# Optimization experiments

Measured on AMD Instinct MI355X. Metric: run time of the kernel, lower is better.

## Reference

```python
import jax, jax.numpy as jnp
import numpy as np

N_NODES = 50000
N_EDGES = 800000
IN_DIM = 128
OUT_DIM = 128
NUM_HEADS = 8
HEAD_DIM = OUT_DIM // NUM_HEADS
LN_EPS = 1e-5


def setup_inputs() -> dict:
    key = jax.random.key(0)
    ks = jax.random.split(key, 8)
    # xavier-uniform bounds
    def xavier(k, shape, fan_in, fan_out):
        a = float(np.sqrt(6.0 / (fan_in + fan_out)))
        return jax.random.uniform(k, shape, jnp.float32, -a, a)
    x = jax.random.normal(ks[0], (N_NODES, IN_DIM), jnp.float32)
    edge_index = jax.random.randint(ks[1], (2, N_EDGES), 0, N_NODES, jnp.int32)
    # store Linear weights as (in, out) so forward is x @ W (same math as torch x @ W.T)
    W_src = xavier(ks[2], (IN_DIM, OUT_DIM), IN_DIM, OUT_DIM)
    W_dst = xavier(ks[3], (IN_DIM, OUT_DIM), IN_DIM, OUT_DIM)
    attn = xavier(ks[4], (NUM_HEADS, HEAD_DIM), HEAD_DIM, NUM_HEADS)
    W_out = xavier(ks[5], (OUT_DIM, OUT_DIM), OUT_DIM, OUT_DIM)
    b_out = jnp.zeros((OUT_DIM,), jnp.float32)
    gamma = jnp.ones((OUT_DIM,), jnp.float32)
    beta = jnp.zeros((OUT_DIM,), jnp.float32)
    return {"x": x, "edge_index": edge_index, "W_src": W_src, "W_dst": W_dst,
            "attn": attn, "W_out": W_out, "b_out": b_out, "gamma": gamma, "beta": beta}


def reference(x, edge_index, W_src, W_dst, attn, W_out, b_out, gamma, beta):
    N = x.shape[0]
    H, D = attn.shape
    src, dst = edge_index[0], edge_index[1]
    # node transforms: (N, H, D)
    h_src = (x @ W_src).reshape(N, H, D)
    h_dst = (x @ W_dst).reshape(N, H, D)
    # per-edge GATv2 attention logits (E, H)
    h_src_e = h_src[src]                                  # (E, H, D)
    e = jax.nn.leaky_relu(h_src_e + h_dst[dst], 0.2)
    s = jnp.einsum('ehd,hd->eh', e, attn)
    # segment (scatter) softmax over incoming edges of each dst node
    m = jax.ops.segment_max(s, dst, num_segments=N)       # (N, H)
    exp = jnp.exp(s - m[dst])
    denom = jax.ops.segment_sum(exp, dst, num_segments=N)
    alpha = exp / (denom[dst] + 1e-8)                     # (E, H)
    # weighted message aggregation
    msg = (h_src_e * alpha[..., None]).reshape(-1, H * D)
    out = jax.ops.segment_sum(msg, dst, num_segments=N)   # (N, H*D)
    out = out @ W_out + b_out
    out = out + x                                          # residual (in_dim == out_dim)
    # LayerNorm
    mu = jnp.mean(out, axis=-1, keepdims=True)
    var = jnp.var(out, axis=-1, keepdims=True)
    out = (out - mu) * jax.lax.rsqrt(var + LN_EPS) * gamma + beta
    return out
```

## Files before the change

### kernel.cpp

```cpp
#include <hip/hip_runtime.h>
#include <hip/hip_bf16.h>

#define HEADS 8
#define CDIM 128
#define CAP 96
#define CHUNK 2048
#define LOG2E 1.44269504088896f

typedef __attribute__((ext_vector_type(8))) short bf16x8;
typedef __attribute__((ext_vector_type(4))) float f32x4;
typedef __attribute__((ext_vector_type(2))) _Float16 h16x2;

__device__ __forceinline__ unsigned short f2bs(float f) {
    union { __hip_bfloat16 b; unsigned short u; } c;
    c.b = __float2bfloat16(f);
    return c.u;
}

__device__ __forceinline__ unsigned short f2hs(float f) {
    union { _Float16 h; unsigned short u; } c;
    c.h = (_Float16)f;
    return c.u;
}

__global__ __launch_bounds__(256) void prep_kernel(
        const int* __restrict__ ei,
        int* __restrict__ cnt,
        int* __restrict__ bucket,
        const float* __restrict__ Wsrc,
        const float* __restrict__ Wdst,
        const float* __restrict__ Wout,
        unsigned short* __restrict__ WT,
        unsigned short* __restrict__ WoT, int E, int nedgeblk) {
    const int b = blockIdx.x;
    if (b < nedgeblk) {
        const int shard = b & 7;
        const int base = (b >> 3) * CHUNK;
        int end = base + CHUNK; if (end > E) end = E;
        for (int e = base + (int)threadIdx.x; e < end; e += 256) {
            const int dst = ei[E + e];
            if ((dst & 7) == shard) {
                const int src = ei[e];
                const int pos = atomicAdd(&cnt[dst], 1);
                if (pos < CAP) bucket[(size_t)dst * CAP + pos] = src;
            }
        }
        return;
    }
    int i = (b - nedgeblk) * 256 + threadIdx.x;
    if (i < 16384)      { WT[i] = f2bs(Wsrc[(i & 127) * CDIM + (i >> 7)]); }
    else if (i < 32768) { int j = i - 16384; WT[16384 + j] = f2bs(Wdst[(j & 127) * CDIM + (j >> 7)]); }
    else if (i < 49152) { int j = i - 32768; WoT[j] = f2bs(Wout[(j & 127) * CDIM + (j >> 7)]); }
}

__global__ __launch_bounds__(256) void transform_mfma64f(
        const float* __restrict__ x,
        const unsigned short* __restrict__ WT,
        unsigned short* __restrict__ hsrc,
        unsigned short* __restrict__ hdst, int N) {
    __shared__ unsigned short As[64][136];
    __shared__ unsigned short Bs[128][136];
    const int t = threadIdx.x;
    const int m0 = blockIdx.x * 64;
    for (int i = t; i < 64 * 32; i += 256) {
        const int r = i >> 5, kq = i & 31;
        const int gr = m0 + r;
        float4 v = make_float4(0.f, 0.f, 0.f, 0.f);
        if (gr < N) v = *(const float4*)(x + (size_t)gr * CDIM + kq * 4);
        uint2 pk;
        pk.x = (unsigned)f2bs(v.x) | ((unsigned)f2bs(v.y) << 16);
        pk.y = (unsigned)f2bs(v.z) | ((unsigned)f2bs(v.w) << 16);
        *(uint2*)&As[r][kq * 4] = pk;
    }
    const int w = t >> 6, lane = t & 63, l16 = lane & 15, quad = lane >> 4;
    const int wm = (w & 1) * 32, wn = (w >> 1) * 64;
#pragma unroll
    for (int half = 0; half < 2; half++) {
        const unsigned short* Wb = WT + (size_t)half * 16384;
        for (int i = t; i < 128 * 16; i += 256) {
            const int r = i >> 4, q = i & 15;
            *(uint4*)&Bs[r][q * 8] = *(const uint4*)(Wb + (size_t)r * CDIM + q * 8);
        }
        __syncthreads();
        f32x4 acc[2][4];
#pragma unroll
        for (int mi = 0; mi < 2; mi++)
#pragma unroll
            for (int ni = 0; ni < 4; ni++) acc[mi][ni] = (f32x4){0.f, 0.f, 0.f, 0.f};
#pragma unroll
        for (int kc = 0; kc < 4; kc++) {
            const int k0 = kc * 32 + quad * 8;
            bf16x8 af[2], bf[4];
            af[0] = *(const bf16x8*)&As[wm + l16][k0];
            af[1] = *(const bf16x8*)&As[wm + 16 + l16][k0];
#pragma unroll
            for (int ni = 0; ni < 4; ni++)
                bf[ni] = *(const bf16x8*)&Bs[wn + ni * 16 + l16][k0];
#pragma unroll
            for (int mi = 0; mi < 2; mi++)
#pragma unroll
                for (int ni = 0; ni < 4; ni++)
                    acc[mi][ni] = __builtin_amdgcn_mfma_f32_16x16x32_bf16(af[mi], bf[ni], acc[mi][ni], 0, 0, 0);
        }
        unsigned short* H = half ? hdst : hsrc;
#pragma unroll
        for (int mi = 0; mi < 2; mi++)
#pragma unroll
            for (int reg = 0; reg < 4; reg++) {
                const int gm = m0 + wm + mi * 16 + quad * 4 + reg;
                if (gm < N) {
#pragma unroll
                    for (int ni = 0; ni < 4; ni++)
                        H[(size_t)gm * CDIM + wn + ni * 16 + l16] = f2hs(acc[mi][ni][reg]);
                }
            }
        __syncthreads();
    }
}

__global__ __launch_bounds__(256) void attn_agg6(
        const unsigned short* __restrict__ hsrc,
        const unsigned short* __restrict__ hdst,
        const float* __restrict__ attn,
        const int* __restrict__ cnt,
        const int* __restrict__ bucket,
        unsigned short* __restrict__ aggb) {
    __shared__ int src_lds[4][CAP];
    const int t = threadIdx.x;
    const int w = t >> 6, lane = t & 63;
    const int dst = blockIdx.x * 4 + w;
    int deg = cnt[dst];
    deg = deg > CAP ? CAP : deg;
    for (int j = lane; j < deg; j += 64)
        src_lds[w][j] = bucket[(size_t)dst * CAP + j];

    const int l32 = lane & 31;
    const int eh = lane >> 5;
    const uint2 hdu = *(const uint2*)(hdst + (size_t)dst * CDIM + l32 * 4);
    const h16x2 hd01 = __builtin_bit_cast(h16x2, hdu.x);
    const h16x2 hd23 = __builtin_bit_cast(h16x2, hdu.y);
    const float4 a4 = ((const float4*)attn)[l32];
    h16x2 a01, a23;
    a01[0] = (_Float16)(a4.x * LOG2E); a01[1] = (_Float16)(a4.y * LOG2E);
    a23[0] = (_Float16)(a4.z * LOG2E); a23[1] = (_Float16)(a4.w * LOG2E);
    const h16x2 k02 = { (_Float16)0.2f, (_Float16)0.2f };

    const unsigned short* hb = hsrc + l32 * 4;

    float l = 0.f, acc0 = 0.f, acc1 = 0.f, acc2 = 0.f, acc3 = 0.f;
    for (int j0 = 0; j0 < deg; j0 += 8) {
        uint2 vv[4];
#pragma unroll
        for (int p = 0; p < 4; p++) {
            const int j = j0 + 2 * p + eh;
            const int sj = (j < deg) ? src_lds[w][j] : 0;
            vv[p] = *(const uint2*)(hb + (size_t)sj * CDIM);
        }
#pragma unroll
        for (int p = 0; p < 4; p++) {
            const int j = j0 + 2 * p + eh;
            const h16x2 v01 = __builtin_bit_cast(h16x2, vv[p].x);
            const h16x2 v23 = __builtin_bit_cast(h16x2, vv[p].y);
            h16x2 e01 = v01 + hd01;
            h16x2 e23 = v23 + hd23;
            e01 = __builtin_elementwise_max(e01, e01 * k02);
            e23 = __builtin_elementwise_max(e23, e23 * k02);
            float pp = __builtin_amdgcn_fdot2(e01, a01, 0.f, false);
            pp = __builtin_amdgcn_fdot2(e23, a23, pp, false);
            pp += __int_as_float(__builtin_amdgcn_update_dpp(0, __float_as_int(pp), 0xB1, 0xF, 0xF, true));
            pp += __int_as_float(__builtin_amdgcn_update_dpp(0, __float_as_int(pp), 0x4E, 0xF, 0xF, true));
            float wgt = __builtin_amdgcn_exp2f(pp);
            wgt = (j < deg) ? wgt : 0.f;
            l += wgt;
            acc0 = fmaf(wgt, (float)v01[0], acc0);
            acc1 = fmaf(wgt, (float)v01[1], acc1);
            acc2 = fmaf(wgt, (float)v23[0], acc2);
            acc3 = fmaf(wgt, (float)v23[1], acc3);
        }
    }
    l    += __shfl_xor(l, 32);
    acc0 += __shfl_xor(acc0, 32);
    acc1 += __shfl_xor(acc1, 32);
    acc2 += __shfl_xor(acc2, 32);
    acc3 += __shfl_xor(acc3, 32);
    if (lane < 32) {
        const float r = 1.f / (l + 1e-8f);
        uint2 o;
        o.x = (unsigned)f2bs(acc0 * r) | ((unsigned)f2bs(acc1 * r) << 16);
        o.y = (unsigned)f2bs(acc2 * r) | ((unsigned)f2bs(acc3 * r) << 16);
        *(uint2*)(aggb + (size_t)dst * CDIM + l32 * 4) = o;
    }
}

__global__ __launch_bounds__(256) void out_mfma_ln64(
        const unsigned short* __restrict__ aggb,
        const float* __restrict__ x,
        const unsigned short* __restrict__ WoT,
        const float* __restrict__ bo,
        const float* __restrict__ gam,
        const float* __restrict__ bet,
        float* __restrict__ out, int N) {
    __shared__ unsigned short As[64][136];
    __shared__ unsigned short Bs[128][136];
    __shared__ float red1[64][2], red2[64][2];
    __shared__ float s_mu[64], s_rs[64];
    const int t = threadIdx.x;
    const int m0 = blockIdx.x * 64;
    for (int i = t; i < 64 * 16; i += 256) {
        const int r = i >> 4, q = i & 15;
        const int gr = m0 + r;
        uint4 v = make_uint4(0u, 0u, 0u, 0u);
        if (gr < N) v = *(const uint4*)(aggb + (size_t)gr * CDIM + q * 8);
        *(uint4*)&As[r][q * 8] = v;
    }
    for (int i = t; i < 128 * 16; i += 256) {
        const int r = i >> 4, q = i & 15;
        *(uint4*)&Bs[r][q * 8] = *(const uint4*)(WoT + (size_t)r * CDIM + q * 8);
    }
    __syncthreads();
    const int w = t >> 6, lane = t & 63, l16 = lane & 15, quad = lane >> 4;
    const int wm = (w & 1) * 32, wn = (w >> 1) * 64;
    f32x4 acc[2][4];
#pragma unroll
    for (int mi = 0; mi < 2; mi++)
#pragma unroll
        for (int ni = 0; ni < 4; ni++) acc[mi][ni] = (f32x4){0.f, 0.f, 0.f, 0.f};
#pragma unroll
    for (int kc = 0; kc < 4; kc++) {
        const int k0 = kc * 32 + quad * 8;
        bf16x8 af[2], bf[4];
        af[0] = *(const bf16x8*)&As[l16 + wm][k0];
        af[1] = *(const bf16x8*)&As[l16 + wm + 16][k0];
#pragma unroll
        for (int ni = 0; ni < 4; ni++)
            bf[ni] = *(const bf16x8*)&Bs[wn + ni * 16 + l16][k0];
#pragma unroll
        for (int mi = 0; mi < 2; mi++)
#pragma unroll
            for (int ni = 0; ni < 4; ni++)
                acc[mi][ni] = __builtin_amdgcn_mfma_f32_16x16x32_bf16(af[mi], bf[ni], acc[mi][ni], 0, 0, 0);
    }
    float bi[4], g4[4], be4[4];
#pragma unroll
    for (int ni = 0; ni < 4; ni++) {
        const int n = wn + ni * 16 + l16;
        bi[ni] = bo[n]; g4[ni] = gam[n]; be4[ni] = bet[n];
    }
#pragma unroll
    for (int mi = 0; mi < 2; mi++)
#pragma unroll
        for (int reg = 0; reg < 4; reg++) {
            const int gm = m0 + wm + mi * 16 + quad * 4 + reg;
#pragma unroll
            for (int ni = 0; ni < 4; ni++) {
                const float xr = (gm < N) ? x[(size_t)gm * CDIM + wn + ni * 16 + l16] : 0.f;
                acc[mi][ni][reg] += bi[ni] + xr;
            }
        }
#pragma unroll
    for (int mi = 0; mi < 2; mi++)
#pragma unroll
        for (int reg = 0; reg < 4; reg++) {
            float s1 = acc[mi][0][reg] + acc[mi][1][reg] + acc[mi][2][reg] + acc[mi][3][reg];
            float s2 = acc[mi][0][reg] * acc[mi][0][reg] + acc[mi][1][reg] * acc[mi][1][reg]
                     + acc[mi][2][reg] * acc[mi][2][reg] + acc[mi][3][reg] * acc[mi][3][reg];
            s1 += __shfl_xor(s1, 1, 16); s1 += __shfl_xor(s1, 2, 16);
            s1 += __shfl_xor(s1, 4, 16); s1 += __shfl_xor(s1, 8, 16);
            s2 += __shfl_xor(s2, 1, 16); s2 += __shfl_xor(s2, 2, 16);
            s2 += __shfl_xor(s2, 4, 16); s2 += __shfl_xor(s2, 8, 16);
            if (l16 == 0) {
                const int row = wm + mi * 16 + quad * 4 + reg;
                red1[row][w >> 1] = s1;
                red2[row][w >> 1] = s2;
            }
        }
    __syncthreads();
    if (t < 64) {
        const float s1 = red1[t][0] + red1[t][1];
        const float s2 = red2[t][0] + red2[t][1];
        const float mu = s1 * (1.f / 128.f);
        const float var = s2 * (1.f / 128.f) - mu * mu;
        s_mu[t] = mu;
        s_rs[t] = rsqrtf(var + 1e-5f);
    }
    __syncthreads();
#pragma unroll
    for (int mi = 0; mi < 2; mi++)
#pragma unroll
        for (int reg = 0; reg < 4; reg++) {
            const int row = wm + mi * 16 + quad * 4 + reg;
            const int gm = m0 + row;
            if (gm < N) {
                const float mu = s_mu[row], rs = s_rs[row];
#pragma unroll
                for (int ni = 0; ni < 4; ni++)
                    out[(size_t)gm * CDIM + wn + ni * 16 + l16] =
                        (acc[mi][ni][reg] - mu) * rs * g4[ni] + be4[ni];
            }
        }
}

extern "C" void kernel_launch(void* const* d_in, const int* in_sizes, int n_in,
                              void* d_out, int out_size, void* d_ws, size_t ws_size,
                              hipStream_t stream) {
    const float* x    = (const float*)d_in[0];
    const int*   ei   = (const int*)d_in[1];
    const float* Wsrc = (const float*)d_in[2];
    const float* Wdst = (const float*)d_in[3];
    const float* attn = (const float*)d_in[4];
    const float* Wout = (const float*)d_in[5];
    const float* bo   = (const float*)d_in[6];
    const float* gam  = (const float*)d_in[7];
    const float* bet  = (const float*)d_in[8];
    float* out = (float*)d_out;

    const int N = in_sizes[0] / CDIM;
    const int E = in_sizes[1] / 2;
    const int NX = N * CDIM;

    unsigned short* hsrc_h = (unsigned short*)d_ws;
    unsigned short* hdst_h = hsrc_h + (size_t)NX;
    unsigned short* aggb   = hdst_h + (size_t)NX;
    unsigned short* WT     = aggb + (size_t)NX;
    unsigned short* WoT    = WT + 32768;
    int* cnt    = (int*)(WoT + 16384);
    int* bucket = cnt + N;

    (void)hipMemsetAsync(cnt, 0, (size_t)N * sizeof(int), stream);

    const int ngroups  = (E + CHUNK - 1) / CHUNK;
    const int nedgeblk = ngroups * 8;
    const int nwblk    = 49152 / 256;
    prep_kernel<<<nedgeblk + nwblk, 256, 0, stream>>>(ei, cnt, bucket, Wsrc, Wdst, Wout, WT, WoT, E, nedgeblk);
    transform_mfma64f<<<(N + 63) / 64, 256, 0, stream>>>(x, WT, hsrc_h, hdst_h, N);
    attn_agg6<<<N / 4, 256, 0, stream>>>(hsrc_h, hdst_h, attn, cnt, bucket, aggb);
    out_mfma_ln64<<<(N + 63) / 64, 256, 0, stream>>>(aggb, x, WoT, bo, gam, bet, out, N);
}
```

Measured before the change: 202.0 us.

## Fuse edge bucketing with node transform GEMM and fold memset into init kernel

Replaces the memset and the prep kernel with a small init kernel that zeroes counts and transposes the weights. Edge bucketing and the bf16 MFMA node transform now run as one launch, interleaved one GEMM block per four bucket blocks. The goal is to overlap the atomic-heavy, latency-bound bucketing with the compute-bound GEMM and to drop one launch. In exchange, every block of the fused kernel reserves the GEMM's shared memory, which can lower occupancy for the bucketing blocks.

```diff
diff --git a/kernel.cpp b/kernel.cpp
--- a/kernel.cpp
+++ b/kernel.cpp
@@ -23,19 +23,41 @@
     return c.u;
 }
 
-__global__ __launch_bounds__(256) void prep_kernel(
-        const int* __restrict__ ei,
+__global__ __launch_bounds__(256) void init_kernel(
         int* __restrict__ cnt,
-        int* __restrict__ bucket,
         const float* __restrict__ Wsrc,
         const float* __restrict__ Wdst,
         const float* __restrict__ Wout,
         unsigned short* __restrict__ WT,
-        unsigned short* __restrict__ WoT, int E, int nedgeblk) {
+        unsigned short* __restrict__ WoT, int N, int nzblk) {
     const int b = blockIdx.x;
-    if (b < nedgeblk) {
-        const int shard = b & 7;
-        const int base = (b >> 3) * CHUNK;
+    if (b < nzblk) {
+        const int i = b * 256 + threadIdx.x;
+        if (i < N) cnt[i] = 0;
+        return;
+    }
+    const int i = (b - nzblk) * 256 + threadIdx.x;
+    if (i < 16384)      { WT[i] = f2bs(Wsrc[(i & 127) * CDIM + (i >> 7)]); }
+    else if (i < 32768) { int j = i - 16384; WT[16384 + j] = f2bs(Wdst[(j & 127) * CDIM + (j >> 7)]); }
+    else if (i < 49152) { int j = i - 32768; WoT[j] = f2bs(Wout[(j & 127) * CDIM + (j >> 7)]); }
+}
+
+__global__ __launch_bounds__(256) void fused_bucket_transform(
+        const int* __restrict__ ei,
+        int* __restrict__ cnt,
+        int* __restrict__ bucket,
+        const float* __restrict__ x,
+        const unsigned short* __restrict__ WT,
+        unsigned short* __restrict__ hsrc,
+        unsigned short* __restrict__ hdst,
+        int N, int E, int ngemm, int nbucket) {
+    const int g = blockIdx.x;
+    const bool is_gemm = ((g % 5) == 4) && ((g / 5) < ngemm);
+    if (!is_gemm) {
+        const int bid = g - g / 5;
+        if (bid >= nbucket) return;
+        const int shard = bid & 7;
+        const int base = (bid >> 3) * CHUNK;
         int end = base + CHUNK; if (end > E) end = E;
         for (int e = base + (int)threadIdx.x; e < end; e += 256) {
             const int dst = ei[E + e];
@@ -47,21 +69,10 @@
         }
         return;
     }
-    int i = (b - nedgeblk) * 256 + threadIdx.x;
-    if (i < 16384)      { WT[i] = f2bs(Wsrc[(i & 127) * CDIM + (i >> 7)]); }
-    else if (i < 32768) { int j = i - 16384; WT[16384 + j] = f2bs(Wdst[(j & 127) * CDIM + (j >> 7)]); }
-    else if (i < 49152) { int j = i - 32768; WoT[j] = f2bs(Wout[(j & 127) * CDIM + (j >> 7)]); }
-}
-
-__global__ __launch_bounds__(256) void transform_mfma64f(
-        const float* __restrict__ x,
-        const unsigned short* __restrict__ WT,
-        unsigned short* __restrict__ hsrc,
-        unsigned short* __restrict__ hdst, int N) {
     __shared__ unsigned short As[64][136];
     __shared__ unsigned short Bs[128][136];
     const int t = threadIdx.x;
-    const int m0 = blockIdx.x * 64;
+    const int m0 = (g / 5) * 64;
     for (int i = t; i < 64 * 32; i += 256) {
         const int r = i >> 5, kq = i & 31;
         const int gr = m0 + r;
@@ -326,13 +337,15 @@
     int* cnt    = (int*)(WoT + 16384);
     int* bucket = cnt + N;
 
-    (void)hipMemsetAsync(cnt, 0, (size_t)N * sizeof(int), stream);
-
+    const int nzblk    = (N + 255) / 256;
+    const int nwblk    = 49152 / 256;
     const int ngroups  = (E + CHUNK - 1) / CHUNK;
-    const int nedgeblk = ngroups * 8;
-    const int nwblk    = 49152 / 256;
-    prep_kernel<<<nedgeblk + nwblk, 256, 0, stream>>>(ei, cnt, bucket, Wsrc, Wdst, Wout, WT, WoT, E, nedgeblk);
-    transform_mfma64f<<<(N + 63) / 64, 256, 0, stream>>>(x, WT, hsrc_h, hdst_h, N);
+    const int nbucket  = ngroups * 8;
+    const int ngemm    = (N + 63) / 64;
+
+    init_kernel<<<nzblk + nwblk, 256, 0, stream>>>(cnt, Wsrc, Wdst, Wout, WT, WoT, N, nzblk);
+    fused_bucket_transform<<<nbucket + ngemm, 256, 0, stream>>>(
+        ei, cnt, bucket, x, WT, hsrc_h, hdst_h, N, E, ngemm, nbucket);
     attn_agg6<<<N / 4, 256, 0, stream>>>(hsrc_h, hdst_h, attn, cnt, bucket, aggb);
     out_mfma_ln64<<<(N + 63) / 64, 256, 0, stream>>>(aggb, x, WoT, bo, gam, bet, out, N);
 }
```

New measurement: 201.6 us. About the same (-0.2%).
